# Optimization experiments

Hardware: AMD Instinct MI355X
Metric: run time of the kernel (lower is better)

Reference implementation:

```python
import math
import jax, jax.numpy as jnp
import numpy as np

B, T, D_MODEL, N_HEADS = 2, 2048, 1024, 16
HEAD_DIM = D_MODEL // N_HEADS  # 64


def setup_inputs() -> dict:
    key = jax.random.key(0)
    k1, k2, k3, k4, k5 = jax.random.split(key, 5)
    x = jax.random.normal(k1, (B, T, D_MODEL), dtype=jnp.float32)
    init = 0.02
    Wq = jax.random.normal(k2, (D_MODEL, D_MODEL), dtype=jnp.float32) * init
    Wk = jax.random.normal(k3, (D_MODEL, D_MODEL), dtype=jnp.float32) * init
    Wv = jax.random.normal(k4, (D_MODEL, D_MODEL), dtype=jnp.float32) * init
    Wo = jax.random.normal(k5, (D_MODEL, D_MODEL), dtype=jnp.float32) * init
    # causal mask, broadcastable over (B, H): 1 = keep, 0 = masked
    mask = jnp.tril(jnp.ones((T, T), dtype=jnp.int32))[None, None, :, :]
    return {"x": x, "Wq": Wq, "Wk": Wk, "Wv": Wv, "Wo": Wo, "mask": mask}


def ternary_weight(W):
    # BitNet-b1.58 style ternary quantization with straight-through estimator
    scale = jnp.mean(jnp.abs(W))
    Wt = jnp.round(jnp.clip(W / (scale + 1e-8), -1.0, 1.0)) * scale
    return W + jax.lax.stop_gradient(Wt - W)


def rope_cos_sin(seq_len, dim):
    inv_freq = 1.0 / (10000.0 ** (jnp.arange(0, dim, 2, dtype=jnp.float32) / dim))
    freqs = jnp.outer(jnp.arange(seq_len, dtype=jnp.float32), inv_freq)  # [T, dim/2]
    emb = jnp.concatenate([freqs, freqs], axis=-1)  # [T, dim]
    return jnp.cos(emb)[None, None, :, :], jnp.sin(emb)[None, None, :, :]


def rotate_half(x):
    h = x.shape[-1] // 2
    return jnp.concatenate([-x[..., h:], x[..., :h]], axis=-1)


def reference(x, Wq, Wk, Wv, Wo, mask):
    Bb, Tt, C = x.shape
    H, D = N_HEADS, HEAD_DIM
    # ternary-quantized projections (bias-free)
    q = (x @ ternary_weight(Wq).T).reshape(Bb, Tt, H, D).transpose(0, 2, 1, 3)
    k = (x @ ternary_weight(Wk).T).reshape(Bb, Tt, H, D).transpose(0, 2, 1, 3)
    v = (x @ ternary_weight(Wv).T).reshape(Bb, Tt, H, D).transpose(0, 2, 1, 3)
    cos, sin = rope_cos_sin(Tt, D)  # [1,1,T,D]
    q = q * cos + rotate_half(q) * sin
    k = k * cos + rotate_half(k) * sin
    att = jnp.einsum("bhqd,bhkd->bhqk", q, k) / math.sqrt(D)
    att = jnp.where(mask == 0, -jnp.inf, att)
    att = jax.nn.softmax(att, axis=-1)  # dropout omitted (eval mode, p effectively 0)
    y = jnp.einsum("bhqk,bhkd->bhqd", att, v)
    y = y.transpose(0, 2, 1, 3).reshape(Bb, Tt, C)
    return y @ ternary_weight(Wo).T
```

## Files before the change

kernel.cpp:

```cpp
#include <hip/hip_runtime.h>
#include <math.h>

using bf16x8  = __attribute__((ext_vector_type(8))) __bf16;
using floatx4 = __attribute__((ext_vector_type(4))) float;
using ushortx8 = __attribute__((ext_vector_type(8))) unsigned short;
using ushortx4 = __attribute__((ext_vector_type(4))) unsigned short;
typedef unsigned short u16;

__device__ __forceinline__ float bf2f(u16 u) {
  unsigned int x = ((unsigned int)u) << 16;
  return __builtin_bit_cast(float, x);
}
__device__ __forceinline__ u16 f2bf(float f) {
  unsigned int x = __builtin_bit_cast(unsigned int, f);
  x += 0x7FFFu + ((x >> 16) & 1u);
  return (u16)(x >> 16);
}
__device__ __forceinline__ float fexp2(float x) { return __builtin_amdgcn_exp2f(x); }
__device__ __forceinline__ unsigned cvtpk(float lo, float hi) {
  unsigned r;
  asm("v_cvt_pk_bf16_f32 %0, %1, %2" : "=v"(r) : "v"(lo), "v"(hi));
  return r;
}

#define GLDS16(SRC, DST)                                                        \
  __builtin_amdgcn_global_load_lds((const __attribute__((address_space(1))) void*)(SRC), \
                                   (__attribute__((address_space(3))) void*)(DST), 16, 0, 0)

__global__ __launch_bounds__(256) void cvt_kernel(const float* __restrict__ x, u16* __restrict__ xb) {
  int g = (blockIdx.x * 256 + threadIdx.x) * 8;
  float4 a = *(const float4*)(x + g);
  float4 b = *(const float4*)(x + g + 4);
  ushortx8 o;
  o[0] = f2bf(a.x); o[1] = f2bf(a.y); o[2] = f2bf(a.z); o[3] = f2bf(a.w);
  o[4] = f2bf(b.x); o[5] = f2bf(b.y); o[6] = f2bf(b.z); o[7] = f2bf(b.w);
  *(ushortx8*)(xb + g) = o;
}

__global__ __launch_bounds__(256) void absum_kernel(const float* W0, const float* W1,
                                                    const float* W2, const float* W3,
                                                    float* partials) {
  const float* W = (blockIdx.y == 0) ? W0 : (blockIdx.y == 1) ? W1 : (blockIdx.y == 2) ? W2 : W3;
  int tid = threadIdx.x;
  int base = blockIdx.x * 16384 + tid;
  float s = 0.f;
#pragma unroll
  for (int i = 0; i < 64; ++i) s += fabsf(W[base + i * 256]);
  __shared__ float red[256];
  red[tid] = s;
  __syncthreads();
  for (int off = 128; off > 0; off >>= 1) {
    if (tid < off) red[tid] += red[tid + off];
    __syncthreads();
  }
  if (tid == 0) partials[blockIdx.y * 64 + blockIdx.x] = red[0];
}

__global__ void scales_kernel(const float* partials, float* scales) {
  int w = threadIdx.x;
  if (w < 4) {
    float s = 0.f;
    for (int i = 0; i < 64; ++i) s += partials[w * 64 + i];
    scales[w] = s * (1.f / 1048576.f);
  }
}

__global__ __launch_bounds__(256) void quant_kernel(const float* W0, const float* W1,
                                                    const float* W2, const float* W3,
                                                    const float* scales, u16* Wt) {
  int w = blockIdx.y;
  const float* W = (w == 0) ? W0 : (w == 1) ? W1 : (w == 2) ? W2 : W3;
  u16* O = Wt + (size_t)w * (1u << 20);
  float s = scales[w] + 1e-8f;
  int e = (blockIdx.x * 256 + threadIdx.x) * 4;
  float4 v = *(const float4*)(W + e);
  ushortx4 o;
  o[0] = f2bf(rintf(fminf(fmaxf(v.x / s, -1.f), 1.f)));
  o[1] = f2bf(rintf(fminf(fmaxf(v.y / s, -1.f), 1.f)));
  o[2] = f2bf(rintf(fminf(fmaxf(v.z / s, -1.f), 1.f)));
  o[3] = f2bf(rintf(fminf(fmaxf(v.w / s, -1.f), 1.f)));
  *(ushortx4*)(O + e) = o;
}

__global__ __launch_bounds__(256) void gemm_qkv(const u16* __restrict__ A, const u16* __restrict__ Wt,
                                                u16* __restrict__ QKV, u16* __restrict__ vt,
                                                const float* __restrict__ scales) {
  const int K = 1024;
  __shared__ __align__(16) u16 As[128][64];
  __shared__ __align__(16) u16 Bs[64][64];
  int tid = threadIdx.x;
  int wave = tid >> 6, lane = tid & 63;
  int quad = lane >> 4, l16 = lane & 15;
  int flat = blockIdx.y * 32 + blockIdx.x;
  int swz = (flat & 7) * 192 + (flat >> 3);
  int bx = swz & 31, by = swz >> 5;
  int bm = bx * 128;
  int bnc = by * 64;
  int mat = bnc >> 10, bn = bnc & 1023;
  int wm = wave * 32;
  floatx4 acc[2][4] = {};
  const u16* ga = A  + (size_t)(bm + wave * 32 + (lane >> 3)) * K + (lane & 7) * 8;
  const u16* gb = Wt + (size_t)(bnc + wave * 16 + (lane >> 3)) * K + (lane & 7) * 8;
  for (int k0 = 0; k0 < K; k0 += 64) {
    __syncthreads();
#pragma unroll
    for (int i = 0; i < 4; ++i)
      GLDS16(ga + (size_t)i * 8 * K + k0, &As[wave * 32 + i * 8][0]);
#pragma unroll
    for (int i = 0; i < 2; ++i)
      GLDS16(gb + (size_t)i * 8 * K + k0, &Bs[wave * 16 + i * 8][0]);
    __syncthreads();
#pragma unroll
    for (int kk = 0; kk < 64; kk += 32) {
      bf16x8 a[2], b[4];
#pragma unroll
      for (int i = 0; i < 2; ++i)
        a[i] = __builtin_bit_cast(bf16x8, *(const ushortx8*)&As[wm + i * 16 + l16][kk + quad * 8]);
#pragma unroll
      for (int j = 0; j < 4; ++j)
        b[j] = __builtin_bit_cast(bf16x8, *(const ushortx8*)&Bs[j * 16 + l16][kk + quad * 8]);
#pragma unroll
      for (int i = 0; i < 2; ++i)
#pragma unroll
        for (int j = 0; j < 4; ++j)
          acc[i][j] = __builtin_amdgcn_mfma_f32_16x16x32_bf16(a[i], b[j], acc[i][j], 0, 0, 0);
    }
  }
  float sc = scales[mat];
  if (mat < 2) {
    u16* outp = QKV + (size_t)mat * (4u << 20);
    float qs = (mat == 0) ? 0.125f * 1.4426950408889634f : 1.0f;
    float inv0 = exp2f(-(float)l16 * (13.287712379549449f / 32.f));
    float inv1 = exp2f(-(float)(16 + l16) * (13.287712379549449f / 32.f));
#pragma unroll
    for (int i = 0; i < 2; ++i)
#pragma unroll
      for (int rg = 0; rg < 4; ++rg) {
        int row = bm + wm + i * 16 + quad * 4 + rg;
        float tf = (float)(row & 2047);
#pragma unroll
        for (int j = 0; j < 2; ++j) {
          float ang = tf * (j ? inv1 : inv0);
          float s = __sinf(ang), c = __cosf(ang);
          float v1 = acc[i][j][rg] * sc, v2 = acc[i][j + 2][rg] * sc;
          int col = bn + j * 16 + l16;
          outp[(size_t)row * 1024 + col]      = f2bf((v1 * c - v2 * s) * qs);
          outp[(size_t)row * 1024 + col + 32] = f2bf((v2 * c + v1 * s) * qs);
        }
      }
  } else {
    int h = bn >> 6;
#pragma unroll
    for (int i = 0; i < 2; ++i) {
      int row0 = bm + wm + i * 16 + quad * 4;
      int b = row0 >> 11, t0 = row0 & 2047;
#pragma unroll
      for (int j = 0; j < 4; ++j) {
        int d = j * 16 + l16;
        ushortx4 o;
#pragma unroll
        for (int rg = 0; rg < 4; ++rg) o[rg] = f2bf(acc[i][j][rg] * sc);
        *(ushortx4*)(vt + (size_t)((b * 16 + h) * 64 + d) * 2048 + t0) = o;
      }
    }
  }
}

__global__ __launch_bounds__(256) void gemm_out(const u16* __restrict__ A, const u16* __restrict__ B,
                                                float* __restrict__ C, const float* __restrict__ scale_ptr) {
  const int K = 1024, N = 1024;
  __shared__ __align__(16) u16 As[128][64];
  __shared__ __align__(16) u16 Bs[128][64];
  int tid = threadIdx.x;
  int wave = tid >> 6, lane = tid & 63;
  int quad = lane >> 4, l16 = lane & 15;
  int bm = blockIdx.x * 128, bn = blockIdx.y * 128;
  int wm = (wave >> 1) * 64, wn = (wave & 1) * 64;
  floatx4 acc[4][4] = {};
  const u16* ga = A + (size_t)(bm + wave * 32 + (lane >> 3)) * K + (lane & 7) * 8;
  const u16* gb = B + (size_t)(bn + wave * 32 + (lane >> 3)) * K + (lane & 7) * 8;
  for (int k0 = 0; k0 < K; k0 += 64) {
    __syncthreads();
#pragma unroll
    for (int i = 0; i < 4; ++i)
      GLDS16(ga + (size_t)i * 8 * K + k0, &As[wave * 32 + i * 8][0]);
#pragma unroll
    for (int i = 0; i < 4; ++i)
      GLDS16(gb + (size_t)i * 8 * K + k0, &Bs[wave * 32 + i * 8][0]);
    __syncthreads();
#pragma unroll
    for (int kk = 0; kk < 64; kk += 32) {
      bf16x8 a[4], b[4];
#pragma unroll
      for (int i = 0; i < 4; ++i)
        a[i] = __builtin_bit_cast(bf16x8, *(const ushortx8*)&As[wm + i * 16 + l16][kk + quad * 8]);
#pragma unroll
      for (int j = 0; j < 4; ++j)
        b[j] = __builtin_bit_cast(bf16x8, *(const ushortx8*)&Bs[wn + j * 16 + l16][kk + quad * 8]);
#pragma unroll
      for (int i = 0; i < 4; ++i)
#pragma unroll
        for (int j = 0; j < 4; ++j)
          acc[i][j] = __builtin_amdgcn_mfma_f32_16x16x32_bf16(a[i], b[j], acc[i][j], 0, 0, 0);
    }
  }
  float sc = scale_ptr[0];
#pragma unroll
  for (int i = 0; i < 4; ++i)
#pragma unroll
    for (int j = 0; j < 4; ++j)
#pragma unroll
      for (int rg = 0; rg < 4; ++rg) {
        int row = bm + wm + i * 16 + quad * 4 + rg;
        int col = bn + wn + j * 16 + l16;
        C[(size_t)row * N + col] = acc[i][j][rg] * sc;
      }
}

__global__ __launch_bounds__(256, 2) void attn_kernel(const u16* __restrict__ q, const u16* __restrict__ k,
                                                      const u16* __restrict__ vt, u16* __restrict__ y) {
  __shared__ __align__(16) u16 Ks[2][64][72];
  __shared__ __align__(16) u16 Vt[2][64][72];
  __shared__ __align__(16) u16 Ps[8][16][72];
  const int T = 2048, C = 1024;
  int tid = threadIdx.x;
  int wave = tid >> 6, lane = tid & 63;
  int quad = lane >> 4, l16 = lane & 15;
  int p = blockIdx.x;
  int b = blockIdx.y >> 4, h = blockIdx.y & 15;
  int wq[2];
  wq[0] = p * 64 + wave * 16;
  wq[1] = (31 - p) * 64 + wave * 16;
  int dt[2] = {p, 31 - p};
  int nkt = 32 - p;

  bf16x8 bq[2][2];
#pragma unroll
  for (int g = 0; g < 2; ++g) {
    const u16* gq = q + (size_t)(b * T + wq[g] + l16) * C + h * 64 + quad * 8;
    bq[g][0] = __builtin_bit_cast(bf16x8, *(const ushortx8*)(gq));
    bq[g][1] = __builtin_bit_cast(bf16x8, *(const ushortx8*)(gq + 32));
  }

  ushortx8 onesu;
#pragma unroll
  for (int j = 0; j < 8; ++j) onesu[j] = 0x3F80;
  bf16x8 bones = __builtin_bit_cast(bf16x8, onesu);

  int srow = tid >> 2, sc16 = (tid & 3) << 4;
  const u16* kptr  = k  + (size_t)(b * T + srow) * C + h * 64 + sc16;
  const u16* vtptr = vt + (size_t)(blockIdx.y * 64 + srow) * 2048 + sc16;

  floatx4 o[2][5] = {};

  ushortx8 kra = *(const ushortx8*)kptr;
  ushortx8 krb = *(const ushortx8*)(kptr + 8);
  ushortx8 vra = *(const ushortx8*)vtptr;
  ushortx8 vrb = *(const ushortx8*)(vtptr + 8);
  *(ushortx8*)&Ks[0][srow][sc16]     = kra;
  *(ushortx8*)&Ks[0][srow][sc16 + 8] = krb;
  *(ushortx8*)&Vt[0][srow][sc16]     = vra;
  *(ushortx8*)&Vt[0][srow][sc16 + 8] = vrb;
  __syncthreads();

  for (int kt = 0; kt < nkt; ++kt) {
    int cur = kt & 1;
    bool haveNext = (kt + 1) < nkt;
    if (haveNext) {
      kra = *(const ushortx8*)(kptr + (size_t)(kt + 1) * 64 * C);
      krb = *(const ushortx8*)(kptr + (size_t)(kt + 1) * 64 * C + 8);
      vra = *(const ushortx8*)(vtptr + (kt + 1) * 64);
      vrb = *(const ushortx8*)(vtptr + (kt + 1) * 64 + 8);
    }

    bool act[2] = {kt <= dt[0], true};

    floatx4 sacc[2][4] = {};
#pragma unroll
    for (int nt = 0; nt < 4; ++nt) {
      bf16x8 ak0 = __builtin_bit_cast(bf16x8, *(const ushortx8*)&Ks[cur][nt * 16 + l16][quad * 8]);
      bf16x8 ak1 = __builtin_bit_cast(bf16x8, *(const ushortx8*)&Ks[cur][nt * 16 + l16][32 + quad * 8]);
#pragma unroll
      for (int g = 0; g < 2; ++g)
        if (act[g]) {
          sacc[g][nt] = __builtin_amdgcn_mfma_f32_16x16x32_bf16(ak0, bq[g][0], sacc[g][nt], 0, 0, 0);
          sacc[g][nt] = __builtin_amdgcn_mfma_f32_16x16x32_bf16(ak1, bq[g][1], sacc[g][nt], 0, 0, 0);
        }
    }

#pragma unroll
    for (int g = 0; g < 2; ++g)
      if (act[g]) {
        if (kt == dt[g]) {
          int qg = wq[g] + l16;
#pragma unroll
          for (int nt = 0; nt < 4; ++nt)
#pragma unroll
            for (int rg = 0; rg < 4; ++rg)
              if (kt * 64 + nt * 16 + quad * 4 + rg > qg) sacc[g][nt][rg] = -__builtin_inff();
        }
#pragma unroll
        for (int nt = 0; nt < 4; ++nt) {
          float p0 = fexp2(sacc[g][nt][0]);
          float p1 = fexp2(sacc[g][nt][1]);
          float p2 = fexp2(sacc[g][nt][2]);
          float p3 = fexp2(sacc[g][nt][3]);
          unsigned lo = cvtpk(p0, p1);
          unsigned hi = cvtpk(p2, p3);
          *(uint2*)&Ps[wave * 2 + g][l16][nt * 16 + quad * 4] = make_uint2(lo, hi);
        }
      }

    bf16x8 ap[2][2];
#pragma unroll
    for (int g = 0; g < 2; ++g)
      if (act[g]) {
        ap[g][0] = __builtin_bit_cast(bf16x8, *(const ushortx8*)&Ps[wave * 2 + g][l16][quad * 8]);
        ap[g][1] = __builtin_bit_cast(bf16x8, *(const ushortx8*)&Ps[wave * 2 + g][l16][32 + quad * 8]);
      }
#pragma unroll
    for (int nt = 0; nt < 4; ++nt) {
      bf16x8 bv0 = __builtin_bit_cast(bf16x8, *(const ushortx8*)&Vt[cur][nt * 16 + l16][quad * 8]);
      bf16x8 bv1 = __builtin_bit_cast(bf16x8, *(const ushortx8*)&Vt[cur][nt * 16 + l16][32 + quad * 8]);
#pragma unroll
      for (int g = 0; g < 2; ++g)
        if (act[g]) {
          o[g][nt] = __builtin_amdgcn_mfma_f32_16x16x32_bf16(ap[g][0], bv0, o[g][nt], 0, 0, 0);
          o[g][nt] = __builtin_amdgcn_mfma_f32_16x16x32_bf16(ap[g][1], bv1, o[g][nt], 0, 0, 0);
        }
    }
#pragma unroll
    for (int g = 0; g < 2; ++g)
      if (act[g]) {
        o[g][4] = __builtin_amdgcn_mfma_f32_16x16x32_bf16(ap[g][0], bones, o[g][4], 0, 0, 0);
        o[g][4] = __builtin_amdgcn_mfma_f32_16x16x32_bf16(ap[g][1], bones, o[g][4], 0, 0, 0);
      }

    if (haveNext) {
      int nb = cur ^ 1;
      *(ushortx8*)&Ks[nb][srow][sc16]     = kra;
      *(ushortx8*)&Ks[nb][srow][sc16 + 8] = krb;
      *(ushortx8*)&Vt[nb][srow][sc16]     = vra;
      *(ushortx8*)&Vt[nb][srow][sc16 + 8] = vrb;
    }
    __syncthreads();
  }

#pragma unroll
  for (int g = 0; g < 2; ++g)
#pragma unroll
    for (int nt = 0; nt < 4; ++nt)
#pragma unroll
      for (int rg = 0; rg < 4; ++rg) {
        int qg = wq[g] + quad * 4 + rg;
        int col = h * 64 + nt * 16 + l16;
        y[(size_t)(b * T + qg) * C + col] = f2bf(o[g][nt][rg] / o[g][4][rg]);
      }
}

extern "C" void kernel_launch(void* const* d_in, const int* in_sizes, int n_in,
                              void* d_out, int out_size, void* d_ws, size_t ws_size,
                              hipStream_t stream) {
  const float* x  = (const float*)d_in[0];
  const float* Wq = (const float*)d_in[1];
  const float* Wk = (const float*)d_in[2];
  const float* Wv = (const float*)d_in[3];
  const float* Wo = (const float*)d_in[4];

  char* ws = (char*)d_ws;
  float* partials = (float*)ws;
  float* scales   = (float*)(ws + 1024);
  u16* Wt  = (u16*)(ws + 4096);
  u16* xb  = (u16*)(ws + 4096 + (size_t)(8u << 20));
  u16* qb  = xb + (4u << 20);
  u16* kb  = qb + (4u << 20);
  u16* vtb = kb + (4u << 20);
  u16* yb  = vtb + (4u << 20);
  float* out = (float*)d_out;

  cvt_kernel<<<2048, 256, 0, stream>>>(x, xb);
  absum_kernel<<<dim3(64, 4), 256, 0, stream>>>(Wq, Wk, Wv, Wo, partials);
  scales_kernel<<<1, 64, 0, stream>>>(partials, scales);
  quant_kernel<<<dim3(1024, 4), 256, 0, stream>>>(Wq, Wk, Wv, Wo, scales, Wt);

  gemm_qkv<<<dim3(32, 48), 256, 0, stream>>>(xb, Wt, qb, vtb, scales);
  attn_kernel<<<dim3(16, 32), 256, 0, stream>>>(qb, kb, vtb, yb);
  gemm_out<<<dim3(32, 8), 256, 0, stream>>>(yb, Wt + 3 * (1u << 20), out, scales + 3);
}
```

Before: 214.8 us.

## Merge prep kernels and fold scale reduction into consumers, cutting launches

Merges the bf16 conversion of x and the per-matrix abs-sum reduction into one launch. Drops the separate scales kernel, so each consumer kernel now sums the 64 partials itself. This removes two kernel launches and their serialization gaps, at the cost of a small redundant 64-element reduction per thread. It also removes the block-index swizzle in the QKV GEMM, which may change L2 locality.

```diff
diff --git a/kernel.cpp b/kernel.cpp
--- a/kernel.cpp
+++ b/kernel.cpp
@@ -22,56 +22,55 @@
   asm("v_cvt_pk_bf16_f32 %0, %1, %2" : "=v"(r) : "v"(lo), "v"(hi));
   return r;
 }
+__device__ __forceinline__ float scale_of(const float* __restrict__ partials, int w) {
+  float s = 0.f;
+  for (int i = 0; i < 64; ++i) s += partials[w * 64 + i];
+  return s * (1.f / 1048576.f);
+}
 
 #define GLDS16(SRC, DST)                                                        \
   __builtin_amdgcn_global_load_lds((const __attribute__((address_space(1))) void*)(SRC), \
                                    (__attribute__((address_space(3))) void*)(DST), 16, 0, 0)
 
-__global__ __launch_bounds__(256) void cvt_kernel(const float* __restrict__ x, u16* __restrict__ xb) {
-  int g = (blockIdx.x * 256 + threadIdx.x) * 8;
-  float4 a = *(const float4*)(x + g);
-  float4 b = *(const float4*)(x + g + 4);
-  ushortx8 o;
-  o[0] = f2bf(a.x); o[1] = f2bf(a.y); o[2] = f2bf(a.z); o[3] = f2bf(a.w);
-  o[4] = f2bf(b.x); o[5] = f2bf(b.y); o[6] = f2bf(b.z); o[7] = f2bf(b.w);
-  *(ushortx8*)(xb + g) = o;
-}
-
-__global__ __launch_bounds__(256) void absum_kernel(const float* W0, const float* W1,
-                                                    const float* W2, const float* W3,
-                                                    float* partials) {
-  const float* W = (blockIdx.y == 0) ? W0 : (blockIdx.y == 1) ? W1 : (blockIdx.y == 2) ? W2 : W3;
+__global__ __launch_bounds__(256) void prep_kernel(const float* __restrict__ x, u16* __restrict__ xb,
+                                                   const float* W0, const float* W1,
+                                                   const float* W2, const float* W3,
+                                                   float* partials) {
+  __shared__ float red[256];
   int tid = threadIdx.x;
-  int base = blockIdx.x * 16384 + tid;
+  if (blockIdx.x < 2048) {
+    int g = (blockIdx.x * 256 + tid) * 8;
+    float4 a = *(const float4*)(x + g);
+    float4 b = *(const float4*)(x + g + 4);
+    ushortx8 o;
+    o[0] = f2bf(a.x); o[1] = f2bf(a.y); o[2] = f2bf(a.z); o[3] = f2bf(a.w);
+    o[4] = f2bf(b.x); o[5] = f2bf(b.y); o[6] = f2bf(b.z); o[7] = f2bf(b.w);
+    *(ushortx8*)(xb + g) = o;
+    return;
+  }
+  int idx = blockIdx.x - 2048;
+  int bx = idx & 63, w = idx >> 6;
+  const float* W = (w == 0) ? W0 : (w == 1) ? W1 : (w == 2) ? W2 : W3;
+  int base = bx * 16384 + tid;
   float s = 0.f;
 #pragma unroll
   for (int i = 0; i < 64; ++i) s += fabsf(W[base + i * 256]);
-  __shared__ float red[256];
   red[tid] = s;
   __syncthreads();
   for (int off = 128; off > 0; off >>= 1) {
     if (tid < off) red[tid] += red[tid + off];
     __syncthreads();
   }
-  if (tid == 0) partials[blockIdx.y * 64 + blockIdx.x] = red[0];
-}
-
-__global__ void scales_kernel(const float* partials, float* scales) {
-  int w = threadIdx.x;
-  if (w < 4) {
-    float s = 0.f;
-    for (int i = 0; i < 64; ++i) s += partials[w * 64 + i];
-    scales[w] = s * (1.f / 1048576.f);
-  }
+  if (tid == 0) partials[w * 64 + bx] = red[0];
 }
 
 __global__ __launch_bounds__(256) void quant_kernel(const float* W0, const float* W1,
                                                     const float* W2, const float* W3,
-                                                    const float* scales, u16* Wt) {
+                                                    const float* partials, u16* Wt) {
   int w = blockIdx.y;
   const float* W = (w == 0) ? W0 : (w == 1) ? W1 : (w == 2) ? W2 : W3;
   u16* O = Wt + (size_t)w * (1u << 20);
-  float s = scales[w] + 1e-8f;
+  float s = scale_of(partials, w) + 1e-8f;
   int e = (blockIdx.x * 256 + threadIdx.x) * 4;
   float4 v = *(const float4*)(W + e);
   ushortx4 o;
@@ -84,18 +83,15 @@
 
 __global__ __launch_bounds__(256) void gemm_qkv(const u16* __restrict__ A, const u16* __restrict__ Wt,
                                                 u16* __restrict__ QKV, u16* __restrict__ vt,
-                                                const float* __restrict__ scales) {
+                                                const float* __restrict__ partials) {
   const int K = 1024;
   __shared__ __align__(16) u16 As[128][64];
   __shared__ __align__(16) u16 Bs[64][64];
   int tid = threadIdx.x;
   int wave = tid >> 6, lane = tid & 63;
   int quad = lane >> 4, l16 = lane & 15;
-  int flat = blockIdx.y * 32 + blockIdx.x;
-  int swz = (flat & 7) * 192 + (flat >> 3);
-  int bx = swz & 31, by = swz >> 5;
-  int bm = bx * 128;
-  int bnc = by * 64;
+  int bm = blockIdx.x * 128;
+  int bnc = blockIdx.y * 64;
   int mat = bnc >> 10, bn = bnc & 1023;
   int wm = wave * 32;
   floatx4 acc[2][4] = {};
@@ -126,7 +122,7 @@
           acc[i][j] = __builtin_amdgcn_mfma_f32_16x16x32_bf16(a[i], b[j], acc[i][j], 0, 0, 0);
     }
   }
-  float sc = scales[mat];
+  float sc = scale_of(partials, mat);
   if (mat < 2) {
     u16* outp = QKV + (size_t)mat * (4u << 20);
     float qs = (mat == 0) ? 0.125f * 1.4426950408889634f : 1.0f;
@@ -167,7 +163,7 @@
 }
 
 __global__ __launch_bounds__(256) void gemm_out(const u16* __restrict__ A, const u16* __restrict__ B,
-                                                float* __restrict__ C, const float* __restrict__ scale_ptr) {
+                                                float* __restrict__ C, const float* __restrict__ partials) {
   const int K = 1024, N = 1024;
   __shared__ __align__(16) u16 As[128][64];
   __shared__ __align__(16) u16 Bs[128][64];
@@ -204,7 +200,7 @@
           acc[i][j] = __builtin_amdgcn_mfma_f32_16x16x32_bf16(a[i], b[j], acc[i][j], 0, 0, 0);
     }
   }
-  float sc = scale_ptr[0];
+  float sc = scale_of(partials, 3);
 #pragma unroll
   for (int i = 0; i < 4; ++i)
 #pragma unroll
@@ -369,7 +365,6 @@
 
   char* ws = (char*)d_ws;
   float* partials = (float*)ws;
-  float* scales   = (float*)(ws + 1024);
   u16* Wt  = (u16*)(ws + 4096);
   u16* xb  = (u16*)(ws + 4096 + (size_t)(8u << 20));
   u16* qb  = xb + (4u << 20);
@@ -378,12 +373,10 @@
   u16* yb  = vtb + (4u << 20);
   float* out = (float*)d_out;
 
-  cvt_kernel<<<2048, 256, 0, stream>>>(x, xb);
-  absum_kernel<<<dim3(64, 4), 256, 0, stream>>>(Wq, Wk, Wv, Wo, partials);
-  scales_kernel<<<1, 64, 0, stream>>>(partials, scales);
-  quant_kernel<<<dim3(1024, 4), 256, 0, stream>>>(Wq, Wk, Wv, Wo, scales, Wt);
-
-  gemm_qkv<<<dim3(32, 48), 256, 0, stream>>>(xb, Wt, qb, vtb, scales);
+  prep_kernel<<<2304, 256, 0, stream>>>(x, xb, Wq, Wk, Wv, Wo, partials);
+  quant_kernel<<<dim3(1024, 4), 256, 0, stream>>>(Wq, Wk, Wv, Wo, partials, Wt);
+
+  gemm_qkv<<<dim3(32, 48), 256, 0, stream>>>(xb, Wt, qb, vtb, partials);
   attn_kernel<<<dim3(16, 32), 256, 0, stream>>>(qb, kb, vtb, yb);
-  gemm_out<<<dim3(32, 8), 256, 0, stream>>>(yb, Wt + 3 * (1u << 20), out, scales + 3);
-}
+  gemm_out<<<dim3(32, 8), 256, 0, stream>>>(yb, Wt + 3 * (1u << 20), out, partials);
+}
```

Measured after the change: 209.1 us. -2.6%, faster.
